# Optimization experiments

Measured on AMD Instinct MI355X. Metric: run time of the kernel, lower is better.

The kernel has to match this reference:

```python
import jax, jax.numpy as jnp
import numpy as np

H = 8  # num_heads, fixed in the module


def setup_inputs() -> dict:
    key = jax.random.key(0)
    ks = jax.random.split(key, 26)
    C = 256          # hidden_dim
    K = 16           # num_corners
    B = 8            # images
    P = 64           # proposals per image
    N = B * P        # total proposals
    Hf = Wf = 14     # feature map HxW (T = 196 keys per proposal)
    Hq = Wq = 10     # query grid (S = 100 queries)
    s = 1.0 / np.sqrt(C)

    def w(k, shape):
        return jax.random.normal(k, shape, jnp.float32) * s

    return {
        "features": jax.random.normal(ks[0], (N, C, Hf, Wf), jnp.float32),
        "query_features": jax.random.normal(ks[1], (B, C, Hq, Wq), jnp.float32),
        # self-attention params (torch MHA: y = x @ W.T + b)
        "wq_s": w(ks[2], (C, C)), "wk_s": w(ks[3], (C, C)), "wv_s": w(ks[4], (C, C)),
        "bq_s": jnp.zeros((C,), jnp.float32), "bk_s": jnp.zeros((C,), jnp.float32), "bv_s": jnp.zeros((C,), jnp.float32),
        "wo_s": w(ks[5], (C, C)), "bo_s": jnp.zeros((C,), jnp.float32),
        # cross-attention params
        "wq_c": w(ks[6], (C, C)), "wk_c": w(ks[7], (C, C)), "wv_c": w(ks[8], (C, C)),
        "bq_c": jnp.zeros((C,), jnp.float32), "bk_c": jnp.zeros((C,), jnp.float32), "bv_c": jnp.zeros((C,), jnp.float32),
        "wo_c": w(ks[9], (C, C)), "bo_c": jnp.zeros((C,), jnp.float32),
        # polygon MLP head
        "w1": w(ks[10], (C, C)), "b1": jnp.zeros((C,), jnp.float32),
        "w2": w(ks[11], (2 * K, C)), "b2": jnp.zeros((2 * K,), jnp.float32),
        # score head
        "ws": w(ks[12], (1, C)), "bs": jnp.zeros((1,), jnp.float32),
    }


def _forward(features, query_features,
             wq_s, wk_s, wv_s, bq_s, bk_s, bv_s, wo_s, bo_s,
             wq_c, wk_c, wv_c, bq_c, bk_c, bv_c, wo_c, bo_c,
             w1, b1, w2, b2, ws, bs):
    B, C = query_features.shape[0], query_features.shape[1]
    dh = C // H
    scale = 1.0 / jnp.sqrt(jnp.asarray(dh, jnp.float32))

    # query_features: (B,C,Hq,Wq) -> (S,B,C)
    qf = query_features.reshape(B, C, -1).transpose(2, 0, 1)
    S = qf.shape[0]

    # ---- self-attention over queries ----
    q = (qf @ wq_s.T + bq_s).reshape(S, B, H, dh)
    k = (qf @ wk_s.T + bk_s).reshape(S, B, H, dh)
    v = (qf @ wv_s.T + bv_s).reshape(S, B, H, dh)
    att = jax.nn.softmax(jnp.einsum('sbhd,tbhd->bhst', q, k) * scale, axis=-1)
    qsa = jnp.einsum('bhst,tbhd->sbhd', att, v).reshape(S, B, C) @ wo_s.T + bo_s  # (S,B,C)

    # features: (N,C,Hf,Wf) -> (B,P,T,C) with T=Hf*Wf, P=N//B
    N = features.shape[0]
    P = N // B
    feats = features.reshape(N, C, -1).transpose(0, 2, 1).reshape(B, P, -1, C)

    # ---- cross-attention: same (S,C) query broadcast over P proposals ----
    qc = (qsa @ wq_c.T + bq_c).reshape(S, B, H, dh)
    kc = (feats @ wk_c.T + bk_c).reshape(B, P, -1, H, dh)
    vc = (feats @ wv_c.T + bv_c).reshape(B, P, -1, H, dh)
    sc = jnp.einsum('sbhd,bpthd->bphst', qc, kc) * scale  # (B,P,H,S,T)
    a = jax.nn.softmax(sc, axis=-1)
    o = jnp.einsum('bphst,bpthd->bpshd', a, vc).reshape(B, P, S, C) @ wo_c.T + bo_c  # (B,P,S,C)

    # ---- heads, then mean over the S query positions ----
    h1 = jax.nn.relu(o @ w1.T + b1)
    polygons = (h1 @ w2.T + b2).mean(axis=2).reshape(N, -1)          # (N, 2K)
    scores = jax.nn.sigmoid(o @ ws.T + bs).mean(axis=2).reshape(N, 1)  # (N, 1)
    return polygons, scores


def reference(features, query_features,
              wq_s, wk_s, wv_s, bq_s, bk_s, bv_s, wo_s, bo_s,
              wq_c, wk_c, wv_c, bq_c, bk_c, bv_c, wo_c, bo_c,
              w1, b1, w2, b2, ws, bs):
    return _forward(features, query_features,
                    wq_s, wk_s, wv_s, bq_s, bk_s, bv_s, wo_s, bo_s,
                    wq_c, wk_c, wv_c, bq_c, bk_c, bv_c, wo_c, bo_c,
                    w1, b1, w2, b2, ws, bs)
```

## Files before the change

### kernel.cpp

```cpp
#include <hip/hip_runtime.h>
#include <hip/hip_bf16.h>


typedef __attribute__((ext_vector_type(8))) short bf16x8;
typedef __attribute__((ext_vector_type(4))) float f32x4;

__device__ __forceinline__ float bf2f(ushort u) {
    union { float f; uint u32; } v; v.u32 = ((uint)u) << 16; return v.f;
}
__device__ __forceinline__ ushort f2bf(float f) {
    union { float f; uint u; } v; v.f = f;
    uint r = v.u + 0x7FFF + ((v.u >> 16) & 1);
    return (ushort)(r >> 16);
}
__device__ __forceinline__ uint pk2(float a, float b) {
    __hip_bfloat162 h = __float22bfloat162_rn(make_float2(a, b));
    union { __hip_bfloat162 h2; uint u; } c; c.h2 = h; return c.u;
}
__device__ __forceinline__ f32x4 MFMA(bf16x8 a, bf16x8 b, f32x4 c) {
    return __builtin_amdgcn_mfma_f32_16x16x32_bf16(a, b, c, 0, 0, 0);
}

#define SCALE_DH 0.17677669529663687f

#define TOTALW (2337 * 256)
#define QCPN   (8 * 8 * 112 * 32)
#define NBIAS  2337

__global__ void prep_kernel(const float* w0, const float* w1_, const float* w2_,
                            const float* w3, const float* w4, const float* w5,
                            const float* w6, const float* w7, const float* w8,
                            const float* w9, const float* w10,
                            const float* b0, const float* b1_, const float* b2_,
                            const float* b3, const float* b4, const float* b5,
                            const float* b6, const float* b7, const float* b8,
                            const float* b9, const float* b10,
                            ushort* wbf, float* bias, ushort* qcp)
{
    for (size_t i = blockIdx.x * blockDim.x + threadIdx.x;
         i < (size_t)TOTALW + QCPN + NBIAS; i += (size_t)gridDim.x * blockDim.x) {
        if (i < TOTALW) {
            int row = (int)(i >> 8), col = (int)(i & 255);
            const float* sp; int base;
            if      (row < 256)  { sp = w0;  base = 0; }
            else if (row < 512)  { sp = w1_; base = 256; }
            else if (row < 768)  { sp = w2_; base = 512; }
            else if (row < 1024) { sp = w3;  base = 768; }
            else if (row < 1280) { sp = w4;  base = 1024; }
            else if (row < 1536) { sp = w5;  base = 1280; }
            else if (row < 1792) { sp = w6;  base = 1536; }
            else if (row < 2048) { sp = w7;  base = 1792; }
            else if (row < 2304) { sp = w8;  base = 2048; }
            else if (row < 2336) { sp = w9;  base = 2304; }
            else                 { sp = w10; base = 2336; }
            wbf[i] = f2bf(sp[(size_t)(row - base) * 256 + col]);
        } else if (i < (size_t)TOTALW + QCPN) {
            qcp[i - TOTALW] = 0;
        } else {
            int idx = (int)(i - TOTALW - QCPN);
            const float* sp; int base;
            if      (idx < 256)  { sp = b0;  base = 0; }
            else if (idx < 512)  { sp = b1_; base = 256; }
            else if (idx < 768)  { sp = b2_; base = 512; }
            else if (idx < 1024) { sp = b3;  base = 768; }
            else if (idx < 1280) { sp = b4;  base = 1024; }
            else if (idx < 1536) { sp = b5;  base = 1280; }
            else if (idx < 1792) { sp = b6;  base = 1536; }
            else if (idx < 2048) { sp = b7;  base = 1792; }
            else if (idx < 2304) { sp = b8;  base = 2048; }
            else if (idx < 2336) { sp = b9;  base = 2304; }
            else                 { sp = b10; base = 2336; }
            bias[idx] = sp[idx - base];
        }
    }
}

template<int ASRC, int GS, int EPI>
__global__ __launch_bounds__(256)
void gemm_rows(const void* Aptr, const ushort* Wall, const float* Ball,
               ushort* Out, int M, int Wrow0, int Brow0, int ldo)
{
    __shared__ ushort As[64 * 40];
    __shared__ ushort Bs[128 * 40];
    int tid = threadIdx.x;
    int lane = tid & 63, w = tid >> 6;
    int lr = lane & 15, lg = lane >> 4;
    int r0 = blockIdx.x * 64;
    int j0 = blockIdx.y * 128;

    f32x4 acc[4][2];
    #pragma unroll
    for (int mt = 0; mt < 4; ++mt)
        #pragma unroll
        for (int nt = 0; nt < 2; ++nt) { f32x4 z = {0.f,0.f,0.f,0.f}; acc[mt][nt] = z; }

    for (int ks = 0; ks < 8; ++ks) {
        int c0 = ks * 32;
        {
            int i = tid >> 2, q = tid & 3;
            int r = r0 + i;
            if (ASRC == 0) {
                uint4 v = make_uint4(0u,0u,0u,0u);
                if (r < M) v = *(const uint4*)((const ushort*)Aptr + (size_t)r * 256 + c0 + q * 8);
                *(uint4*)(&As[i * 40 + q * 8]) = v;
            } else {
                uint u[4] = {0u,0u,0u,0u};
                if (r < M) {
                    int g = r / GS, o = r - g * GS;
                    const float* src = (const float*)Aptr + (size_t)g * 256 * GS + o;
                    #pragma unroll
                    for (int k2 = 0; k2 < 4; ++k2) {
                        ushort a0 = f2bf(src[(size_t)(c0 + q * 8 + 2 * k2)     * GS]);
                        ushort a1 = f2bf(src[(size_t)(c0 + q * 8 + 2 * k2 + 1) * GS]);
                        u[k2] = (uint)a0 | ((uint)a1 << 16);
                    }
                }
                *(uint4*)(&As[i * 40 + q * 8]) = make_uint4(u[0], u[1], u[2], u[3]);
            }
        }
        {
            int jj = tid >> 1, half = tid & 1;
            const ushort* src = Wall + (size_t)(Wrow0 + j0 + jj) * 256 + c0 + half * 16;
            ushort* dst = &Bs[jj * 40 + half * 16];
            *(uint4*)(dst)     = *(const uint4*)(src);
            *(uint4*)(dst + 8) = *(const uint4*)(src + 8);
        }
        __syncthreads();
        bf16x8 bfr[2];
        #pragma unroll
        for (int nt = 0; nt < 2; ++nt)
            bfr[nt] = *(const bf16x8*)(&Bs[(w * 32 + nt * 16 + lr) * 40 + lg * 8]);
        #pragma unroll
        for (int mt = 0; mt < 4; ++mt) {
            bf16x8 afr = *(const bf16x8*)(&As[(mt * 16 + lr) * 40 + lg * 8]);
            acc[mt][0] = MFMA(afr, bfr[0], acc[mt][0]);
            acc[mt][1] = MFMA(afr, bfr[1], acc[mt][1]);
        }
        __syncthreads();
    }
    #pragma unroll
    for (int mt = 0; mt < 4; ++mt) {
        #pragma unroll
        for (int nt = 0; nt < 2; ++nt) {
            int jc = j0 + w * 32 + nt * 16 + lr;
            float bias = Ball[Brow0 + jc];
            #pragma unroll
            for (int rg = 0; rg < 4; ++rg) {
                int r = r0 + mt * 16 + lg * 4 + rg;
                if (r >= M) continue;
                float vv = acc[mt][nt][rg] + bias;
                if (EPI == 0) {
                    Out[(size_t)r * ldo + jc] = f2bf(vv);
                } else {
                    int b = r / 100, s = r - b * 100;
                    int h = jc >> 5, d = jc & 31;
                    Out[(((size_t)(b * 8 + h)) * 112 + s) * 32 + d] = f2bf(vv * SCALE_DH);
                }
            }
        }
    }
}

__global__ __launch_bounds__(128)
void self_attn(const ushort* qkv, ushort* sav)
{
    __shared__ float kls[100][33];
    __shared__ float vls[100][33];
    __shared__ float sls[100][101];
    int bh = blockIdx.x; int b = bh >> 3, h = bh & 7;
    int tid = threadIdx.x;
    for (int idx = tid; idx < 100 * 32; idx += 128) {
        int t = idx >> 5, d = idx & 31;
        kls[t][d] = bf2f(qkv[((size_t)(b * 100 + t)) * 768 + 256 + h * 32 + d]);
        vls[t][d] = bf2f(qkv[((size_t)(b * 100 + t)) * 768 + 512 + h * 32 + d]);
    }
    __syncthreads();
    if (tid < 100) {
        int s = tid;
        float q[32];
        #pragma unroll
        for (int d = 0; d < 32; ++d)
            q[d] = bf2f(qkv[((size_t)(b * 100 + s)) * 768 + h * 32 + d]) * SCALE_DH;
        float mx = -1e30f;
        for (int t = 0; t < 100; ++t) {
            float sc = 0.f;
            #pragma unroll
            for (int d = 0; d < 32; ++d) sc += q[d] * kls[t][d];
            sls[s][t] = sc; mx = fmaxf(mx, sc);
        }
        float sum = 0.f;
        for (int t = 0; t < 100; ++t) {
            float p = __expf(sls[s][t] - mx);
            sls[s][t] = p; sum += p;
        }
        float inv = 1.f / sum;
        float acc2[32];
        #pragma unroll
        for (int d = 0; d < 32; ++d) acc2[d] = 0.f;
        for (int t = 0; t < 100; ++t) {
            float pv = sls[s][t];
            #pragma unroll
            for (int d = 0; d < 32; ++d) acc2[d] += pv * vls[t][d];
        }
        #pragma unroll
        for (int d = 0; d < 32; ++d)
            sav[((size_t)(b * 100 + s)) * 256 + h * 32 + d] = f2bf(acc2[d] * inv);
    }
}

__global__ __launch_bounds__(512, 2)
void kvproj(const float* features, const ushort* Wall, const float* Ball,
            ushort* kc, ushort* vc, int n_base)
{
    __shared__ ushort featT[224 * 264];
    int tid = threadIdx.x;
    int lane = tid & 63, w = tid >> 6;
    int lr = lane & 15, lg = lane >> 4;
    int nl = blockIdx.x;
    int n  = n_base + nl;
    const float* fb = features + (size_t)n * 256 * 196;

    bf16x8 af[4][8];
    #pragma unroll
    for (int m = 0; m < 4; ++m) {
        int row = ((m < 2) ? 1280 : 1536) + w * 32 + (m & 1) * 16 + lr;
        #pragma unroll
        for (int ks = 0; ks < 8; ++ks)
            af[m][ks] = *(const bf16x8*)(Wall + (size_t)row * 256 + ks * 32 + lg * 8);
    }
    float biask0 = Ball[1280 + w * 32 + lr];
    float biask1 = Ball[1296 + w * 32 + lr];
    float biasv0 = Ball[1536 + w * 32 + lr];
    float biasv1 = Ball[1552 + w * 32 + lr];

    #pragma unroll
    for (int it = 0; it < 7; ++it) {
        int idx = tid + it * 512;
        if (idx < 3136) {
            int cg = idx / 49, tq = idx - cg * 49;
            const float* p = fb + (size_t)(cg * 4) * 196 + tq * 4;
            float4 v0 = *(const float4*)(p);
            float4 v1 = *(const float4*)(p + 196);
            float4 v2 = *(const float4*)(p + 392);
            float4 v3 = *(const float4*)(p + 588);
            #pragma unroll
            for (int j = 0; j < 4; ++j) {
                float e0 = (j == 0) ? v0.x : (j == 1) ? v0.y : (j == 2) ? v0.z : v0.w;
                float e1 = (j == 0) ? v1.x : (j == 1) ? v1.y : (j == 2) ? v1.z : v1.w;
                float e2 = (j == 0) ? v2.x : (j == 1) ? v2.y : (j == 2) ? v2.z : v2.w;
                float e3 = (j == 0) ? v3.x : (j == 1) ? v3.y : (j == 2) ? v3.z : v3.w;
                uint2 pr;
                pr.x = pk2(e0, e1);
                pr.y = pk2(e2, e3);
                *(uint2*)(&featT[(tq * 4 + j) * 264 + cg * 4]) = pr;
            }
        }
    }
    for (int idx = tid; idx < 12 * 264; idx += 512)
        featT[196 * 264 + idx] = 0;
    __syncthreads();

    for (int tt = 0; tt < 13; ++tt) {
        bf16x8 a8[8];
        #pragma unroll
        for (int ks = 0; ks < 8; ++ks)
            a8[ks] = *(const bf16x8*)(&featT[(tt * 16 + lr) * 264 + ks * 32 + lg * 8]);
        f32x4 acc[4];
        #pragma unroll
        for (int m = 0; m < 4; ++m) { f32x4 z = {0.f,0.f,0.f,0.f}; acc[m] = z; }
        #pragma unroll
        for (int ks = 0; ks < 8; ++ks)
            #pragma unroll
            for (int m = 0; m < 4; ++m)
                acc[m] = MFMA(a8[ks], af[m][ks], acc[m]);

        int tb = tt * 16 + lg * 4;
        #pragma unroll
        for (int rg = 0; rg < 4; ++rg) {
            int t = tb + rg;
            if (t < 196) {
                kc[((size_t)nl * 224 + t) * 256 + w * 32 + lr]      = f2bf(acc[0][rg] + biask0);
                kc[((size_t)nl * 224 + t) * 256 + w * 32 + 16 + lr] = f2bf(acc[1][rg] + biask1);
            }
        }
        if (tb < 196) {
            size_t vb0 = ((size_t)nl * 256 + w * 32 + lr) * 224 + tb;
            size_t vb1 = ((size_t)nl * 256 + w * 32 + 16 + lr) * 224 + tb;
            uint a01 = pk2(acc[2][0] + biasv0, acc[2][1] + biasv0);
            uint a23 = pk2(acc[2][2] + biasv0, acc[2][3] + biasv0);
            uint b01 = pk2(acc[3][0] + biasv1, acc[3][1] + biasv1);
            uint b23 = pk2(acc[3][2] + biasv1, acc[3][3] + biasv1);
            *(uint*)(vc + vb0)     = a01;
            *(uint*)(vc + vb0 + 2) = a23;
            *(uint*)(vc + vb1)     = b01;
            *(uint*)(vc + vb1 + 2) = b23;
        }
    }
}

__global__ __launch_bounds__(512, 2)
void attn_fuse(const ushort* qcp, const ushort* kc, const ushort* vc,
               const ushort* Wall, const float* Ball, float* outp, int n_base)
{
    __shared__ char smem[130816];
    ushort* OL  = (ushort*)smem;
    float* hbar = (float*)(smem + 59392);
    float* scb  = (float*)(smem + 60416);
    ushort* O2  = (ushort*)(smem + 71680);
    ushort* Pp  = (ushort*)(smem + 71680);

    int tid = threadIdx.x;
    int lane = tid & 63; int w = tid >> 6;
    int lr = lane & 15, lg = lane >> 4;
    int nl = blockIdx.x; int n = n_base + nl;
    int b = n >> 6;
    const ushort* kcn = kc + (size_t)nl * 224 * 256;
    const ushort* vcn = vc + (size_t)nl * 256 * 224;
    ushort* Pw = Pp + w * 640;

    bf16x8 qf[7];
    #pragma unroll
    for (int mt = 0; mt < 7; ++mt)
        qf[mt] = *(const bf16x8*)(qcp + ((((size_t)(b * 8 + w)) * 112 + mt * 16 + lr) * 32 + lg * 8));

    bf16x8 ones;
    #pragma unroll
    for (int j = 0; j < 8; ++j) ones[j] = (short)0x3F80;

    f32x4 o_acc[7][2], l_acc[7];
    #pragma unroll
    for (int mt = 0; mt < 7; ++mt) {
        f32x4 z = {0.f,0.f,0.f,0.f};
        o_acc[mt][0] = z; o_acc[mt][1] = z; l_acc[mt] = z;
    }

    const ushort* kbase = kcn + (size_t)lr * 256 + w * 32 + lg * 8;
    const ushort* vbase = vcn + ((size_t)(w * 32 + lr)) * 224 + lg * 8;

    bf16x8 ck0, ck1, cv0, cv1;
    ck0 = *(const bf16x8*)(kbase);
    ck1 = *(const bf16x8*)(kbase + 16 * 256);
    cv0 = *(const bf16x8*)(vbase);
    cv1 = *(const bf16x8*)(vbase + 16 * 224);

    for (int ch = 0; ch < 7; ++ch) {
        int t0 = ch * 32;
        bf16x8 nk0, nk1, nv0, nv1;
        if (ch < 6) {
            int t0n = t0 + 32;
            nk0 = *(const bf16x8*)(kbase + (size_t)t0n * 256);
            nk1 = *(const bf16x8*)(kbase + (size_t)(t0n + 16) * 256);
            nv0 = *(const bf16x8*)(vbase + t0n);
            nv1 = *(const bf16x8*)(vbase + 16 * 224 + t0n);
            if (t0n == 192) {
                #pragma unroll
                for (int j = 0; j < 8; ++j) {
                    bool inv = (lg * 8 + j) >= 4;
                    nv0[j] = inv ? (short)0 : nv0[j];
                    nv1[j] = inv ? (short)0 : nv1[j];
                }
            }
        }
        bool mask0 = (t0 + lr)      >= 196;
        bool mask1 = (t0 + 16 + lr) >= 196;
        #pragma unroll
        for (int mt = 0; mt < 7; ++mt) {
            f32x4 z = {0.f,0.f,0.f,0.f};
            f32x4 s0 = MFMA(qf[mt], ck0, z);
            f32x4 s1 = MFMA(qf[mt], ck1, z);
            #pragma unroll
            for (int r = 0; r < 4; ++r) {
                float p0 = mask0 ? 0.f : __expf(s0[r]);
                float p1 = mask1 ? 0.f : __expf(s1[r]);
                Pw[(lg * 4 + r) * 40 + lr]      = f2bf(p0);
                Pw[(lg * 4 + r) * 40 + 16 + lr] = f2bf(p1);
            }
            bf16x8 pf = *(const bf16x8*)(&Pw[lr * 40 + lg * 8]);
            o_acc[mt][0] = MFMA(pf, cv0, o_acc[mt][0]);
            o_acc[mt][1] = MFMA(pf, cv1, o_acc[mt][1]);
            l_acc[mt]    = MFMA(pf, ones, l_acc[mt]);
        }
        ck0 = nk0; ck1 = nk1; cv0 = nv0; cv1 = nv1;
    }

    __syncthreads();
    #pragma unroll
    for (int mt = 0; mt < 7; ++mt) {
        #pragma unroll
        for (int r = 0; r < 4; ++r) {
            float inv = 1.f / l_acc[mt][r];
            int srow = mt * 16 + lg * 4 + r;
            OL[srow * 264 + w * 32 + lr]      = f2bf(o_acc[mt][0][r] * inv);
            OL[srow * 264 + w * 32 + 16 + lr] = f2bf(o_acc[mt][1][r] * inv);
        }
    }
    __syncthreads();

    {
        f32x4 a2[7][2];
        #pragma unroll
        for (int mt = 0; mt < 7; ++mt)
            #pragma unroll
            for (int nt = 0; nt < 2; ++nt) { f32x4 z = {0.f,0.f,0.f,0.f}; a2[mt][nt] = z; }
        for (int ks = 0; ks < 8; ++ks) {
            int c0 = ks * 32;
            bf16x8 bw[2];
            #pragma unroll
            for (int nt = 0; nt < 2; ++nt)
                bw[nt] = *(const bf16x8*)(Wall + (size_t)(1792 + w * 32 + nt * 16 + lr) * 256 + c0 + lg * 8);
            #pragma unroll
            for (int mt = 0; mt < 7; ++mt) {
                bf16x8 af = *(const bf16x8*)(&OL[(mt * 16 + lr) * 264 + c0 + lg * 8]);
                a2[mt][0] = MFMA(af, bw[0], a2[mt][0]);
                a2[mt][1] = MFMA(af, bw[1], a2[mt][1]);
            }
        }
        #pragma unroll
        for (int mt = 0; mt < 7; ++mt)
            #pragma unroll
            for (int nt = 0; nt < 2; ++nt) {
                float bias = Ball[1792 + w * 32 + nt * 16 + lr];
                #pragma unroll
                for (int r = 0; r < 4; ++r) {
                    int srow = mt * 16 + lg * 4 + r;
                    O2[srow * 264 + w * 32 + nt * 16 + lr] = f2bf(a2[mt][nt][r] + bias);
                }
            }
    }
    __syncthreads();

    {
        f32x4 a2[7][2];
        #pragma unroll
        for (int mt = 0; mt < 7; ++mt)
            #pragma unroll
            for (int nt = 0; nt < 2; ++nt) { f32x4 z = {0.f,0.f,0.f,0.f}; a2[mt][nt] = z; }
        for (int ks = 0; ks < 8; ++ks) {
            int c0 = ks * 32;
            bf16x8 bw[2];
            #pragma unroll
            for (int nt = 0; nt < 2; ++nt)
                bw[nt] = *(const bf16x8*)(Wall + (size_t)(2048 + w * 32 + nt * 16 + lr) * 256 + c0 + lg * 8);
            #pragma unroll
            for (int mt = 0; mt < 7; ++mt) {
                bf16x8 af = *(const bf16x8*)(&O2[(mt * 16 + lr) * 264 + c0 + lg * 8]);
                a2[mt][0] = MFMA(af, bw[0], a2[mt][0]);
                a2[mt][1] = MFMA(af, bw[1], a2[mt][1]);
            }
        }
        __syncthreads();
        #pragma unroll
        for (int mt = 0; mt < 7; ++mt)
            #pragma unroll
            for (int nt = 0; nt < 2; ++nt) {
                float bias = Ball[2048 + w * 32 + nt * 16 + lr];
                #pragma unroll
                for (int r = 0; r < 4; ++r) {
                    int srow = mt * 16 + lg * 4 + r;
                    float v = a2[mt][nt][r] + bias;
                    v = v > 0.f ? v : 0.f;
                    OL[srow * 264 + w * 32 + nt * 16 + lr] = f2bf(v);
                }
            }
    }
    __syncthreads();

    if (tid < 256) {
        float s = 0.f;
        for (int srow = 0; srow < 100; ++srow) s += bf2f(OL[srow * 264 + tid]);
        hbar[tid] = s * 0.01f;
    }
    if (tid < 100) {
        float s = 0.f;
        for (int c2 = 0; c2 < 256; ++c2)
            s += bf2f(O2[tid * 264 + c2]) * bf2f(Wall[(size_t)2336 * 256 + c2]);
        s += Ball[2336];
        scb[tid] = 1.f / (1.f + __expf(-s));
    }
    __syncthreads();
    if (tid < 32) {
        float s = 0.f;
        for (int c2 = 0; c2 < 256; ++c2)
            s += hbar[c2] * bf2f(Wall[(size_t)(2304 + tid) * 256 + c2]);
        s += Ball[2304 + tid];
        outp[(size_t)n * 32 + tid] = s;
    }
    if (tid == 64) {
        float s = 0.f;
        for (int i2 = 0; i2 < 100; ++i2) s += scb[i2];
        outp[16384 + n] = s * 0.01f;
    }
}

extern "C" void kernel_launch(void* const* d_in, const int* in_sizes, int n_in,
                              void* d_out, int out_size, void* d_ws, size_t ws_size,
                              hipStream_t stream)
{
    const float* features = (const float*)d_in[0];
    const float* qfeat    = (const float*)d_in[1];
    char* ws = (char*)d_ws;

    ushort* wbf  = (ushort*)ws;
    float*  bias = (float*)(ws + 1196544);
    ushort* qkv  = (ushort*)(ws + 1206016);
    ushort* sav  = (ushort*)(ws + 2434816);
    ushort* osb  = (ushort*)(ws + 2844416);
    ushort* qcp  = (ushort*)(ws + 3254016);
    ushort* kvb  = (ushort*)(ws + 3712768);

    prep_kernel<<<dim3(512), dim3(256), 0, stream>>>(
        (const float*)d_in[2], (const float*)d_in[3], (const float*)d_in[4],
        (const float*)d_in[8], (const float*)d_in[10], (const float*)d_in[11],
        (const float*)d_in[12], (const float*)d_in[16], (const float*)d_in[18],
        (const float*)d_in[20], (const float*)d_in[22],
        (const float*)d_in[5], (const float*)d_in[6], (const float*)d_in[7],
        (const float*)d_in[9], (const float*)d_in[13], (const float*)d_in[14],
        (const float*)d_in[15], (const float*)d_in[17], (const float*)d_in[19],
        (const float*)d_in[21], (const float*)d_in[23],
        wbf, bias, qcp);

    gemm_rows<1, 100, 0><<<dim3(13, 6), dim3(256), 0, stream>>>(
        qfeat, wbf, bias, qkv, 800, 0, 0, 768);
    self_attn<<<dim3(64), dim3(128), 0, stream>>>(qkv, sav);
    gemm_rows<0, 1, 0><<<dim3(13, 2), dim3(256), 0, stream>>>(
        sav, wbf, bias, osb, 800, 768, 768, 256);
    gemm_rows<0, 1, 1><<<dim3(13, 2), dim3(256), 0, stream>>>(
        osb, wbf, bias, qcp, 800, 1024, 1024, 0);

    const size_t per_n = 229376;
    long avail = (long)ws_size - 3712768L;
    int Np = 512;
    if (avail < (long)(per_n * 512)) {
        Np = (int)(avail / (long)per_n);
        if (Np < 1) Np = 1;
    }
    ushort* kcb = kvb;
    ushort* vcb = kvb + (size_t)Np * 224 * 256;
    float* outp = (float*)d_out;
    for (int n0 = 0; n0 < 512; n0 += Np) {
        int cnt = (512 - n0 < Np) ? (512 - n0) : Np;
        kvproj<<<dim3(cnt), dim3(512), 0, stream>>>(features, wbf, bias, kcb, vcb, n0);
        attn_fuse<<<dim3(cnt), dim3(512), 0, stream>>>(qcp, kcb, vcb, wbf, bias, outp, n0);
    }
}
```

Measured before the change: 210.4 us.

## Keep attention probabilities in registers by transposing score MFMA operands

The score MFMA now takes K as the A operand and Q as the B operand, so each lane's output already matches the A-operand layout needed by the P·V MFMA. This removes the per-tile round trip of probabilities through LDS and the barrier before the epilogue. V is loaded as split 4-element chunks so that its k-index ordering matches the permuted P layout, and the masking is adjusted to the new token indexing. The cost is more, smaller global loads for V and a more intricate index mapping that has to stay correct.

Result: no change. 206.8 us, median of 2 (-1.7%).

```diff
diff --git a/kernel.cpp b/kernel.cpp
--- a/kernel.cpp
+++ b/kernel.cpp
@@ -307,7 +307,6 @@
     float* hbar = (float*)(smem + 59392);
     float* scb  = (float*)(smem + 60416);
     ushort* O2  = (ushort*)(smem + 71680);
-    ushort* Pp  = (ushort*)(smem + 71680);
 
     int tid = threadIdx.x;
     int lane = tid & 63; int w = tid >> 6;
@@ -316,7 +315,6 @@
     int b = n >> 6;
     const ushort* kcn = kc + (size_t)nl * 224 * 256;
     const ushort* vcn = vc + (size_t)nl * 256 * 224;
-    ushort* Pw = Pp + w * 640;
 
     bf16x8 qf[7];
     #pragma unroll
@@ -335,55 +333,71 @@
     }
 
     const ushort* kbase = kcn + (size_t)lr * 256 + w * 32 + lg * 8;
-    const ushort* vbase = vcn + ((size_t)(w * 32 + lr)) * 224 + lg * 8;
-
-    bf16x8 ck0, ck1, cv0, cv1;
+    const ushort* vb0 = vcn + ((size_t)(w * 32 + lr)) * 224;
+    const ushort* vb1 = vcn + ((size_t)(w * 32 + 16 + lr)) * 224;
+
+    bf16x8 ck0, ck1;
+    uint2 v0lo, v0hi, v1lo, v1hi;
     ck0 = *(const bf16x8*)(kbase);
     ck1 = *(const bf16x8*)(kbase + 16 * 256);
-    cv0 = *(const bf16x8*)(vbase);
-    cv1 = *(const bf16x8*)(vbase + 16 * 224);
+    v0lo = *(const uint2*)(vb0 + 4 * lg);
+    v0hi = *(const uint2*)(vb0 + 16 + 4 * lg);
+    v1lo = *(const uint2*)(vb1 + 4 * lg);
+    v1hi = *(const uint2*)(vb1 + 16 + 4 * lg);
 
     for (int ch = 0; ch < 7; ++ch) {
         int t0 = ch * 32;
-        bf16x8 nk0, nk1, nv0, nv1;
+        bf16x8 nk0, nk1;
+        uint2 n0lo, n0hi, n1lo, n1hi;
         if (ch < 6) {
             int t0n = t0 + 32;
             nk0 = *(const bf16x8*)(kbase + (size_t)t0n * 256);
             nk1 = *(const bf16x8*)(kbase + (size_t)(t0n + 16) * 256);
-            nv0 = *(const bf16x8*)(vbase + t0n);
-            nv1 = *(const bf16x8*)(vbase + 16 * 224 + t0n);
+            n0lo = *(const uint2*)(vb0 + t0n + 4 * lg);
+            n0hi = *(const uint2*)(vb0 + t0n + 16 + 4 * lg);
+            n1lo = *(const uint2*)(vb1 + t0n + 4 * lg);
+            n1hi = *(const uint2*)(vb1 + t0n + 16 + 4 * lg);
             if (t0n == 192) {
-                #pragma unroll
-                for (int j = 0; j < 8; ++j) {
-                    bool inv = (lg * 8 + j) >= 4;
-                    nv0[j] = inv ? (short)0 : nv0[j];
-                    nv1[j] = inv ? (short)0 : nv1[j];
-                }
-            }
-        }
-        bool mask0 = (t0 + lr)      >= 196;
-        bool mask1 = (t0 + 16 + lr) >= 196;
+                uint2 zz = make_uint2(0u, 0u);
+                n0hi = zz; n1hi = zz;
+                if (lg) { n0lo = zz; n1lo = zz; }
+            }
+        }
+        union { uint4 q; bf16x8 v; } u0, u1;
+        u0.q = make_uint4(v0lo.x, v0lo.y, v0hi.x, v0hi.y);
+        u1.q = make_uint4(v1lo.x, v1lo.y, v1hi.x, v1hi.y);
+        bool mA[4], mB[4];
+        #pragma unroll
+        for (int r = 0; r < 4; ++r) {
+            mA[r] = (t0 + 4 * lg + r)      >= 196;
+            mB[r] = (t0 + 16 + 4 * lg + r) >= 196;
+        }
         #pragma unroll
         for (int mt = 0; mt < 7; ++mt) {
             f32x4 z = {0.f,0.f,0.f,0.f};
-            f32x4 s0 = MFMA(qf[mt], ck0, z);
-            f32x4 s1 = MFMA(qf[mt], ck1, z);
-            #pragma unroll
-            for (int r = 0; r < 4; ++r) {
-                float p0 = mask0 ? 0.f : __expf(s0[r]);
-                float p1 = mask1 ? 0.f : __expf(s1[r]);
-                Pw[(lg * 4 + r) * 40 + lr]      = f2bf(p0);
-                Pw[(lg * 4 + r) * 40 + 16 + lr] = f2bf(p1);
-            }
-            bf16x8 pf = *(const bf16x8*)(&Pw[lr * 40 + lg * 8]);
-            o_acc[mt][0] = MFMA(pf, cv0, o_acc[mt][0]);
-            o_acc[mt][1] = MFMA(pf, cv1, o_acc[mt][1]);
-            l_acc[mt]    = MFMA(pf, ones, l_acc[mt]);
-        }
-        ck0 = nk0; ck1 = nk1; cv0 = nv0; cv1 = nv1;
-    }
-
-    __syncthreads();
+            f32x4 s0 = MFMA(ck0, qf[mt], z);
+            f32x4 s1 = MFMA(ck1, qf[mt], z);
+            float p00 = mA[0] ? 0.f : __expf(s0[0]);
+            float p01 = mA[1] ? 0.f : __expf(s0[1]);
+            float p02 = mA[2] ? 0.f : __expf(s0[2]);
+            float p03 = mA[3] ? 0.f : __expf(s0[3]);
+            float p10 = mB[0] ? 0.f : __expf(s1[0]);
+            float p11 = mB[1] ? 0.f : __expf(s1[1]);
+            float p12 = mB[2] ? 0.f : __expf(s1[2]);
+            float p13 = mB[3] ? 0.f : __expf(s1[3]);
+            union { uint4 q; bf16x8 v; } pu;
+            pu.q.x = pk2(p00, p01);
+            pu.q.y = pk2(p02, p03);
+            pu.q.z = pk2(p10, p11);
+            pu.q.w = pk2(p12, p13);
+            o_acc[mt][0] = MFMA(pu.v, u0.v, o_acc[mt][0]);
+            o_acc[mt][1] = MFMA(pu.v, u1.v, o_acc[mt][1]);
+            l_acc[mt]    = MFMA(pu.v, ones, l_acc[mt]);
+        }
+        ck0 = nk0; ck1 = nk1;
+        v0lo = n0lo; v0hi = n0hi; v1lo = n1lo; v1hi = n1hi;
+    }
+
     #pragma unroll
     for (int mt = 0; mt < 7; ++mt) {
         #pragma unroll
```
